# Kernel optimization log

Hardware: AMD Instinct MI355X
Metric: run time of the kernel (lower is better)

The kernel has to match this reference:

```python
import jax, jax.numpy as jnp
import numpy as np

D_INPUT, D_MODEL, D_STATE, D_DISCR, KER = 1024, 2048, 16, 128, 4

def setup_inputs() -> dict:
    key = jax.random.key(0)
    ks = jax.random.split(key, 10)
    sc = lambda fan_in: 1.0 / np.sqrt(fan_in)
    seq = jax.random.normal(ks[0], (2, 1024, D_INPUT), dtype=jnp.float32)
    W_in = jax.random.uniform(ks[1], (2 * D_MODEL, D_INPUT), jnp.float32, -sc(D_INPUT), sc(D_INPUT))
    W_out = jax.random.uniform(ks[2], (D_INPUT, D_MODEL), jnp.float32, -sc(D_MODEL), sc(D_MODEL))
    W_sB = jax.random.uniform(ks[3], (D_STATE, D_MODEL), jnp.float32, -sc(D_MODEL), sc(D_MODEL))
    W_sC = jax.random.uniform(ks[4], (D_STATE, D_MODEL), jnp.float32, -sc(D_MODEL), sc(D_MODEL))
    W_sD1 = jax.random.uniform(ks[5], (D_DISCR, D_MODEL), jnp.float32, -sc(D_MODEL), sc(D_MODEL))
    W_sD2 = jax.random.uniform(ks[6], (D_MODEL, D_DISCR), jnp.float32, -sc(D_DISCR), sc(D_DISCR))
    conv_w = jax.random.uniform(ks[7], (D_MODEL, 1, KER), jnp.float32, -sc(KER), sc(KER))
    conv_b = jax.random.uniform(ks[8], (D_MODEL,), jnp.float32, -sc(KER), sc(KER))
    A_param = jnp.tile(jnp.arange(1, D_STATE + 1, dtype=jnp.float32), (D_MODEL, 1))
    D_param = jnp.ones((D_MODEL,), dtype=jnp.float32)
    return dict(seq=seq, W_in=W_in, W_out=W_out, W_sB=W_sB, W_sC=W_sC,
                W_sD1=W_sD1, W_sD2=W_sD2, conv_w=conv_w, conv_b=conv_b,
                A_param=A_param, D_param=D_param)

def _mamba_fwd(seq, W_in, W_out, W_sB, W_sC, W_sD1, W_sD2, conv_w, conv_b, A_param, D_param):
    b, l, _ = seq.shape
    ab = seq @ W_in.T                                   # [b,l,2*dm]
    a, g = jnp.split(ab, 2, axis=-1)
    # causal depthwise conv: torch pads ker-1 both sides then trims [..., :l]
    x = jnp.swapaxes(a, 1, 2)                           # [b,dm,l]
    y = jax.lax.conv_general_dilated(
        x, conv_w, window_strides=(1,), padding=[(KER - 1, 0)],
        dimension_numbers=('NCH', 'OIH', 'NCH'), feature_group_count=D_MODEL)
    y = y + conv_b[None, :, None]
    a = jax.nn.silu(jnp.swapaxes(y, 1, 2))              # [b,l,dm]
    # SSM
    B = a @ W_sB.T                                      # [b,l,s]
    C = a @ W_sC.T                                      # [b,l,s]
    s_delta = jax.nn.softplus(D_param + (a @ W_sD1.T) @ W_sD2.T)  # [b,l,dm]
    expA = jnp.exp(-A_param)                            # [dm,s]
    A_bar = expA[None, None] * s_delta[..., None]       # [b,l,dm,s]
    X_bar = B[:, :, None, :] * s_delta[..., None] * a[..., None]  # [b,l,dm,s]
    A_t = jnp.moveaxis(A_bar, 1, 0)                     # [l,b,dm,s]
    X_t = jnp.moveaxis(X_bar, 1, 0)
    h0 = jnp.zeros((b, D_MODEL, D_STATE), dtype=seq.dtype)
    def step(h, ax):
        At, Xt = ax
        h = At * h + Xt
        return h, h
    _, hid = jax.lax.scan(step, h0, (A_t, X_t))         # hid: [l,b,dm,s]
    out_ssm = jnp.einsum('lbds,lbs->lbd', hid, jnp.moveaxis(C, 1, 0))
    out_ssm = jnp.moveaxis(out_ssm, 0, 1) + D_param * a # [b,l,dm]
    out = (out_ssm * jax.nn.silu(g)) @ W_out.T          # [b,l,d_input]
    return out

def reference(seq, W_in, W_out, W_sB, W_sC, W_sD1, W_sD2, conv_w, conv_b, A_param, D_param):
    return _mamba_fwd(seq, W_in, W_out, W_sB, W_sC, W_sD1, W_sD2, conv_w, conv_b, A_param, D_param)
```

## Files before the change

kernel.cpp:

```cpp
#include <hip/hip_runtime.h>
#include <math.h>

#define DI 1024
#define DM 2048
#define DS 16
#define LSEQ 1024
#define NB 2
#define NTOK (NB * LSEQ)
#define TC 128
#define WU 32
#define LDU 164
#define NRP 161
#define ZLD 68

typedef unsigned short ushort_t;
typedef __attribute__((ext_vector_type(8))) short short8;
typedef __attribute__((ext_vector_type(4))) float f32x4;

__device__ __forceinline__ float bf2f(ushort_t u) {
    union { unsigned u; float f; } c; c.u = (unsigned)u << 16; return c.f;
}
__device__ __forceinline__ ushort_t f2bf(float f) {
    union { float f; unsigned u; } c; c.f = f;
    unsigned r = c.u + 0x7FFFu + ((c.u >> 16) & 1u);
    return (ushort_t)(r >> 16);
}

__device__ __forceinline__ void gload16(const void* g, void* l) {
    __builtin_amdgcn_global_load_lds(
        (const __attribute__((address_space(1))) void*)g,
        (__attribute__((address_space(3))) void*)l, 16, 0, 0);
}

template<int CTRL>
__device__ __forceinline__ float dpp_mv(float v) {
    int r = __builtin_amdgcn_update_dpp(0, __builtin_bit_cast(int, v), CTRL, 0xF, 0xF, true);
    return __builtin_bit_cast(float, r);
}
__device__ __forceinline__ float sum4(float v) {
    v += dpp_mv<0xB1>(v);
    v += dpp_mv<0x4E>(v);
    return v;
}

__device__ __forceinline__ void cvt4(const float* __restrict__ in,
                                     ushort_t* __restrict__ out, int q) {
    float4 v = ((const float4*)in)[q];
    ushort4 o;
    o.x = f2bf(v.x); o.y = f2bf(v.y); o.z = f2bf(v.z); o.w = f2bf(v.w);
    ((ushort4*)out)[q] = o;
}

__global__ __launch_bounds__(256) void prep(
    const float* __restrict__ seq, const float* __restrict__ W_in,
    const float* __restrict__ W_out, const float* __restrict__ W_sD2,
    const float* __restrict__ Wb, const float* __restrict__ Wc,
    const float* __restrict__ Wd1,
    ushort_t* __restrict__ seq_bf, ushort_t* __restrict__ W_in_bf,
    ushort_t* __restrict__ W_out_bf, ushort_t* __restrict__ W_sD2_bf,
    ushort_t* __restrict__ wbcd)
{
    int q = blockIdx.x * 256 + threadIdx.x;
    if (q < 524288)        cvt4(seq,   seq_bf,   q);
    else if (q < 1572864)  cvt4(W_in,  W_in_bf,  q - 524288);
    else if (q < 2097152)  cvt4(W_out, W_out_bf, q - 1572864);
    else if (q < 2162688)  cvt4(W_sD2, W_sD2_bf, q - 2097152);
    else {
        int p = q - 2162688;
        int idx = p * 4;
        int row = idx >> 11, col = idx & (DM - 1);
        float4 v = make_float4(0.f, 0.f, 0.f, 0.f);
        if (row < 16)       v = *(const float4*)&Wb[row * DM + col];
        else if (row < 32)  v = *(const float4*)&Wc[(row - 16) * DM + col];
        else if (row < 160) v = *(const float4*)&Wd1[(row - 32) * DM + col];
        ushort4 o;
        o.x = f2bf(v.x); o.y = f2bf(v.y); o.z = f2bf(v.z); o.w = f2bf(v.w);
        ((ushort4*)wbcd)[p] = o;
    }
}

template<int TM, int EPI>
__global__ __launch_bounds__(256) void gemm_bt(
    const ushort_t* __restrict__ A, const ushort_t* __restrict__ B,
    void* __restrict__ Cout, int K, int lda, int ldb, int ldc,
    const float* __restrict__ bias, void* __restrict__ Cpart, size_t pstride)
{
    constexpr int MF = TM / 32;
    constexpr int ASZ = TM * 32;
    constexpr int BSZ = 128 * 32;
    __shared__ ushort_t As[2 * ASZ];
    __shared__ ushort_t Bs[2 * BSZ];
    const int tid = threadIdx.x;
    const int lane = tid & 63;
    const int wv = tid >> 6;
    const int wr = wv >> 1, wc = wv & 1;

    const int gx = gridDim.x, gy = gridDim.y;
    const int nwg = gx * gy;
    const int orig = blockIdx.y * gx + blockIdx.x;
    const int q8 = nwg >> 3, r8 = nwg & 7;
    const int xcd = orig & 7, i8 = orig >> 3;
    const int wg = ((xcd < r8) ? xcd * (q8 + 1) : r8 * (q8 + 1) + (xcd - r8) * q8) + i8;
    const int bm = (wg / gx) * TM, bn = (wg % gx) * 128;

    int kbeg = 0, kend = K;
    if (EPI == 5) { int ks = K / gridDim.z; kbeg = blockIdx.z * ks; kend = kbeg + ks; }

    f32x4 acc[MF][4];
#pragma unroll
    for (int m = 0; m < MF; ++m)
#pragma unroll
        for (int n = 0; n < 4; ++n) acc[m][n] = (f32x4){0.f, 0.f, 0.f, 0.f};

    const int r_lo = lane >> 2;
    const int s_l = lane & 3;
    const int row0 = wv * 16 + r_lo;
    const int row1 = 64 + wv * 16 + r_lo;
    const int sg0 = s_l ^ ((row0 >> 1) & 3);
    const int sg1 = s_l ^ ((row1 >> 1) & 3);
    const ushort_t* gA0 = A + (size_t)(bm + row0) * lda + sg0 * 8;
    const ushort_t* gA1 = A + (size_t)(bm + row1) * lda + sg1 * 8;
    const ushort_t* gB0 = B + (size_t)(bn + row0) * ldb + sg0 * 8;
    const ushort_t* gB1 = B + (size_t)(bn + row1) * ldb + sg1 * 8;
    const int lA0o = (wv * 16) * 32;
    const int lA1o = ((TM == 128 ? 64 : 0) + wv * 16) * 32;
    const int lB0o = (wv * 16) * 32;
    const int lB1o = (64 + wv * 16) * 32;

    gload16(gA0 + kbeg, &As[lA0o]);
    if (TM == 128) gload16(gA1 + kbeg, &As[lA1o]);
    gload16(gB0 + kbeg, &Bs[lB0o]);
    gload16(gB1 + kbeg, &Bs[lB1o]);
    __syncthreads();

    int cur = 0;
    for (int k = kbeg; k < kend; k += 32) {
        const int nxt = cur ^ 1;
        if (k + 32 < kend) {
            gload16(gA0 + k + 32, &As[nxt * ASZ + lA0o]);
            if (TM == 128) gload16(gA1 + k + 32, &As[nxt * ASZ + lA1o]);
            gload16(gB0 + k + 32, &Bs[nxt * BSZ + lB0o]);
            gload16(gB1 + k + 32, &Bs[nxt * BSZ + lB1o]);
        }
        const int ca = cur * ASZ, cb = cur * BSZ;
        short8 af[MF], bfr[4];
#pragma unroll
        for (int m = 0; m < MF; ++m) {
            int row = wr * (TM / 2) + m * 16 + (lane & 15);
            int sl = (lane >> 4) ^ ((row >> 1) & 3);
            af[m] = *(const short8*)&As[ca + row * 32 + sl * 8];
        }
#pragma unroll
        for (int n = 0; n < 4; ++n) {
            int row = wc * 64 + n * 16 + (lane & 15);
            int sl = (lane >> 4) ^ ((row >> 1) & 3);
            bfr[n] = *(const short8*)&Bs[cb + row * 32 + sl * 8];
        }
#pragma unroll
        for (int m = 0; m < MF; ++m)
#pragma unroll
            for (int n = 0; n < 4; ++n)
                acc[m][n] = __builtin_amdgcn_mfma_f32_16x16x32_bf16(af[m], bfr[n], acc[m][n], 0, 0, 0);
        __syncthreads();
        cur = nxt;
    }

    const int orow = bm + wr * (TM / 2) + ((lane >> 4) << 2);
    const int ocol = bn + wc * 64 + (lane & 15);
#pragma unroll
    for (int m = 0; m < MF; ++m)
#pragma unroll
        for (int n = 0; n < 4; ++n) {
            int col = ocol + n * 16;
#pragma unroll
            for (int r = 0; r < 4; ++r) {
                int row = orow + m * 16 + r;
                float v = acc[m][n][r];
                if (EPI == 3) {
                    v += bias[col];
                    v = (v > 20.f) ? v : log1pf(__expf(v));
                    ((ushort_t*)Cout)[(size_t)row * ldc + col] = f2bf(v);
                } else if (EPI == 1) {
                    ((ushort_t*)Cout)[(size_t)row * ldc + col] = f2bf(v);
                } else if (EPI == 5) {
                    ((ushort_t*)Cpart + (size_t)blockIdx.z * pstride)[(size_t)row * ldc + col] = f2bf(v);
                } else {
                    ((float*)Cout)[(size_t)row * ldc + col] = v;
                }
            }
        }
}

__global__ __launch_bounds__(256) void reduce_bcd(const ushort_t* __restrict__ part,
                                                  ushort_t* __restrict__ outh)
{
    int q = blockIdx.x * 256 + threadIdx.x;
    float sx = 0.f, sy = 0.f, sz = 0.f, sw = 0.f;
#pragma unroll
    for (int z = 0; z < 8; ++z) {
        ushort4 v = ((const ushort4*)part)[q + z * 131072];
        sx += bf2f(v.x); sy += bf2f(v.y); sz += bf2f(v.z); sw += bf2f(v.w);
    }
    ushort4 o;
    o.x = f2bf(sx); o.y = f2bf(sy); o.z = f2bf(sz); o.w = f2bf(sw);
    ((ushort4*)outh)[q] = o;
}

__global__ __launch_bounds__(256) void reduce_out(const ushort_t* __restrict__ part,
                                                  float* __restrict__ out)
{
    int q = blockIdx.x * 256 + threadIdx.x;
    float sx = 0.f, sy = 0.f, sz = 0.f, sw = 0.f;
#pragma unroll
    for (int z = 0; z < 4; ++z) {
        ushort4 v = ((const ushort4*)part)[q + z * 524288];
        sx += bf2f(v.x); sy += bf2f(v.y); sz += bf2f(v.z); sw += bf2f(v.w);
    }
    float4 o; o.x = sx; o.y = sy; o.z = sz; o.w = sw;
    ((float4*)out)[q] = o;
}

__global__ __launch_bounds__(256) void conv_silu(const ushort_t* __restrict__ ab,
                                                 const float* __restrict__ w,
                                                 const float* __restrict__ bias,
                                                 ushort_t* __restrict__ outh) {
    const int bt = blockIdx.x;
    const int b = bt >> 10, t = bt & (LSEQ - 1);
    const int d = threadIdx.x * 8;

    float wv[8][4];
#pragma unroll
    for (int j = 0; j < 8; ++j) {
        float4 tw = *(const float4*)&w[(d + j) * 4];
        wv[j][0] = tw.x; wv[j][1] = tw.y; wv[j][2] = tw.z; wv[j][3] = tw.w;
    }
    float accv[8];
    {
        float4 b0 = *(const float4*)&bias[d];
        float4 b1 = *(const float4*)&bias[d + 4];
        accv[0] = b0.x; accv[1] = b0.y; accv[2] = b0.z; accv[3] = b0.w;
        accv[4] = b1.x; accv[5] = b1.y; accv[6] = b1.z; accv[7] = b1.w;
    }
#pragma unroll
    for (int k = 0; k < 4; ++k) {
        int tt = t + k - 3;
        if (tt >= 0) {
            short8 av = *(const short8*)&ab[(size_t)(b * LSEQ + tt) * (2 * DM) + d];
#pragma unroll
            for (int j = 0; j < 8; ++j)
                accv[j] = fmaf(bf2f((ushort_t)av[j]), wv[j][k], accv[j]);
        }
    }
    short8 o;
#pragma unroll
    for (int j = 0; j < 8; ++j) {
        float s = accv[j] / (1.f + __expf(-accv[j]));
        o[j] = (short)f2bf(s);
    }
    *(short8*)&outh[(size_t)bt * DM + d] = o;
}

__global__ __launch_bounds__(256) void scan_win(
    const ushort_t* __restrict__ sdel, const ushort_t* __restrict__ aconv,
    const ushort_t* __restrict__ bcd1, const ushort_t* __restrict__ ab,
    const float* __restrict__ A_param, const float* __restrict__ D_param,
    ushort_t* __restrict__ z)
{
    __shared__ ushort_t Ssh[64 * LDU];
    __shared__ ushort_t Vsh[64 * LDU];
    __shared__ float    Bq[4 * NRP * 4];
    __shared__ float    Cq[4 * NRP * 4];
    __shared__ ushort_t Zsh[TC * ZLD];

    const int tid = threadIdx.x;
    const int d0 = blockIdx.x * 64;
    const int c = blockIdx.y, b = blockIdx.z;
    const int nw = (c == 0) ? 0 : WU;
    const int nrows = nw + TC;
    const int tok0 = b * LSEQ + c * TC - nw;
    const int tokout0 = b * LSEQ + c * TC;

    for (int j = tid; j < (nrows / 4) * 32; j += 256) {
        int a = j & 1;
        int r = j >> 1;
        int cq = (r & 15) * 4;
        int row4 = (r >> 4) * 4;
        const ushort_t* src = (a ? aconv : sdel) + (size_t)(tok0 + row4) * DM + d0 + cq;
        ushort4 v0 = *(const ushort4*)(src);
        ushort4 v1 = *(const ushort4*)(src + DM);
        ushort4 v2 = *(const ushort4*)(src + 2 * DM);
        ushort4 v3 = *(const ushort4*)(src + 3 * DM);
        ushort_t* dst = (a ? Vsh : Ssh) + row4;
        *(ushort4*)(dst + (cq + 0) * LDU) = make_ushort4(v0.x, v1.x, v2.x, v3.x);
        *(ushort4*)(dst + (cq + 1) * LDU) = make_ushort4(v0.y, v1.y, v2.y, v3.y);
        *(ushort4*)(dst + (cq + 2) * LDU) = make_ushort4(v0.z, v1.z, v2.z, v3.z);
        *(ushort4*)(dst + (cq + 3) * LDU) = make_ushort4(v0.w, v1.w, v2.w, v3.w);
    }
    for (int j = tid; j < nrows * 8; j += 256) {
        int row = j >> 3, p = j & 7, g = p & 3;
        const ushort_t* src = bcd1 + (size_t)(tok0 + row) * 256 + ((p < 4) ? 4 * g : 16 + 4 * g);
        ushort4 v = *(const ushort4*)src;
        float4 f = make_float4(bf2f(v.x), bf2f(v.y), bf2f(v.z), bf2f(v.w));
        float* dst = ((p < 4) ? Bq : Cq) + (g * NRP + row) * 4;
        *(float4*)dst = f;
    }
    __syncthreads();

    const int q = tid & 3, dl = tid >> 2;
    const int d = d0 + dl;
    float4 av4 = *(const float4*)&A_param[d * DS + 4 * q];
    const float ea0 = __expf(-av4.x), ea1 = __expf(-av4.y);
    const float ea2 = __expf(-av4.z), ea3 = __expf(-av4.w);
    const float Dp = D_param[d];
    float h0 = 0.f, h1 = 0.f, h2 = 0.f, h3 = 0.f;

#define SCAN_STEP_WU(SD, AV, BI) {                                    \
        float sd = (SD), x = sd * (AV);                               \
        float4 Bv = *(const float4*)&Bq[(q * NRP + (BI)) * 4];        \
        h0 = fmaf(sd * ea0, h0, x * Bv.x);                           \
        h1 = fmaf(sd * ea1, h1, x * Bv.y);                           \
        h2 = fmaf(sd * ea2, h2, x * Bv.z);                           \
        h3 = fmaf(sd * ea3, h3, x * Bv.w); }

    for (int i4 = 0; i4 < nw; i4 += 4) {
        ushort4 sdv = *(const ushort4*)&Ssh[dl * LDU + i4];
        ushort4 avv = *(const ushort4*)&Vsh[dl * LDU + i4];
        SCAN_STEP_WU(bf2f(sdv.x), bf2f(avv.x), i4 + 0);
        SCAN_STEP_WU(bf2f(sdv.y), bf2f(avv.y), i4 + 1);
        SCAN_STEP_WU(bf2f(sdv.z), bf2f(avv.z), i4 + 2);
        SCAN_STEP_WU(bf2f(sdv.w), bf2f(avv.w), i4 + 3);
    }

#define SCAN_STEP_OUT(SD, AV, BI, RV) {                               \
        float sd = (SD), av_ = (AV), x = sd * av_;                    \
        float4 Bv = *(const float4*)&Bq[(q * NRP + (BI)) * 4];        \
        float4 Cv = *(const float4*)&Cq[(q * NRP + (BI)) * 4];        \
        h0 = fmaf(sd * ea0, h0, x * Bv.x);                           \
        h1 = fmaf(sd * ea1, h1, x * Bv.y);                           \
        h2 = fmaf(sd * ea2, h2, x * Bv.z);                           \
        h3 = fmaf(sd * ea3, h3, x * Bv.w);                           \
        float r = h0 * Cv.x;                                          \
        r = fmaf(h1, Cv.y, r); r = fmaf(h2, Cv.z, r);                 \
        r = fmaf(h3, Cv.w, r);                                        \
        r = sum4(r);                                                  \
        RV = fmaf(Dp, av_, r); }

    for (int i4 = nw; i4 < nrows; i4 += 4) {
        ushort4 sdv = *(const ushort4*)&Ssh[dl * LDU + i4];
        ushort4 avv = *(const ushort4*)&Vsh[dl * LDU + i4];
        float rv0, rv1, rv2, rv3;
        SCAN_STEP_OUT(bf2f(sdv.x), bf2f(avv.x), i4 + 0, rv0);
        SCAN_STEP_OUT(bf2f(sdv.y), bf2f(avv.y), i4 + 1, rv1);
        SCAN_STEP_OUT(bf2f(sdv.z), bf2f(avv.z), i4 + 2, rv2);
        SCAN_STEP_OUT(bf2f(sdv.w), bf2f(avv.w), i4 + 3, rv3);
        float rvq = (q == 0) ? rv0 : (q == 1) ? rv1 : (q == 2) ? rv2 : rv3;
        int io = i4 - nw;
        Zsh[(io + q) * ZLD + dl] = f2bf(rvq);
    }
    __syncthreads();
    for (int j = tid; j < TC * 16; j += 256) {
        int row = j >> 4, cq = (j & 15) * 4;
        ushort4 ov = *(const ushort4*)&Zsh[row * ZLD + cq];
        ushort4 gv = *(const ushort4*)&ab[(size_t)(tokout0 + row) * (2 * DM) + DM + d0 + cq];
        ushort4 o;
        float g0 = bf2f(gv.x), g1 = bf2f(gv.y), g2 = bf2f(gv.z), g3 = bf2f(gv.w);
        o.x = f2bf(bf2f(ov.x) * (g0 / (1.f + __expf(-g0))));
        o.y = f2bf(bf2f(ov.y) * (g1 / (1.f + __expf(-g1))));
        o.z = f2bf(bf2f(ov.z) * (g2 / (1.f + __expf(-g2))));
        o.w = f2bf(bf2f(ov.w) * (g3 / (1.f + __expf(-g3))));
        *(ushort4*)&z[(size_t)(tokout0 + row) * DM + d0 + cq] = o;
    }
#undef SCAN_STEP_WU
#undef SCAN_STEP_OUT
}

extern "C" void kernel_launch(void* const* d_in, const int* in_sizes, int n_in,
                              void* d_out, int out_size, void* d_ws, size_t ws_size,
                              hipStream_t stream) {
    const float* seq    = (const float*)d_in[0];
    const float* W_in   = (const float*)d_in[1];
    const float* W_out  = (const float*)d_in[2];
    const float* W_sB   = (const float*)d_in[3];
    const float* W_sC   = (const float*)d_in[4];
    const float* W_sD1  = (const float*)d_in[5];
    const float* W_sD2  = (const float*)d_in[6];
    const float* conv_w = (const float*)d_in[7];
    const float* conv_b = (const float*)d_in[8];
    const float* A_par  = (const float*)d_in[9];
    const float* D_par  = (const float*)d_in[10];
    float* out = (float*)d_out;

    char* ws = (char*)d_ws;
    const size_t MiB = 1024 * 1024;
    ushort_t* ab_bf    = (ushort_t*)(ws);
    ushort_t* part_out = (ushort_t*)(ws);
    ushort_t* aconv_h  = (ushort_t*)(ws + 16 * MiB);
    ushort_t* sdel_h   = (ushort_t*)(ws + 24 * MiB);
    ushort_t* W_out_bf = (ushort_t*)(ws + 32 * MiB);
    ushort_t* bcd1     = (ushort_t*)(ws + 36 * MiB);
    ushort_t* W_sD2_bf = (ushort_t*)(ws + 37 * MiB);
    ushort_t* Wbcd     = (ushort_t*)(ws + 37 * MiB + 512*1024);
    ushort_t* seq_bf   = (ushort_t*)(ws + 39 * MiB);
    ushort_t* W_in_bf  = (ushort_t*)(ws + 43 * MiB);
    ushort_t* partK    = (ushort_t*)(ws + 43 * MiB);
    ushort_t* z_bf     = (ushort_t*)(ws + 63 * MiB);

    dim3 blk(256);

    prep<<<dim3(8960), blk, 0, stream>>>(seq, W_in, W_out, W_sD2, W_sB, W_sC, W_sD1,
                                         seq_bf, W_in_bf, W_out_bf, W_sD2_bf, Wbcd);

    gemm_bt<64, 1><<<dim3(32, 32), blk, 0, stream>>>(seq_bf, W_in_bf, ab_bf, 1024, DI, DI, 2 * DM, nullptr, nullptr, 0);

    conv_silu<<<dim3(NTOK), blk, 0, stream>>>(ab_bf, conv_w, conv_b, aconv_h);

    gemm_bt<64, 5><<<dim3(2, 32, 8), blk, 0, stream>>>(aconv_h, Wbcd, nullptr, DM, DM, DM, 256, nullptr, partK, 2048 * 256);

    reduce_bcd<<<dim3(512), blk, 0, stream>>>(partK, bcd1);

    gemm_bt<64, 3><<<dim3(16, 32), blk, 0, stream>>>(bcd1 + 32, W_sD2_bf, sdel_h, 128, 256, 128, DM, D_par, nullptr, 0);

    scan_win<<<dim3(DM / 64, LSEQ / TC, NB), blk, 0, stream>>>(
        sdel_h, aconv_h, bcd1, ab_bf, A_par, D_par, z_bf);

    gemm_bt<64, 5><<<dim3(8, 32, 4), blk, 0, stream>>>(z_bf, W_out_bf, nullptr, DM, DM, DM, DI, nullptr, part_out, 2048 * 1024);

    reduce_out<<<dim3(2048), blk, 0, stream>>>(part_out, out);
}
```

Before: 138.5 us.

## Fuse split-K partial reduction into delta GEMM A-load and scan B/C load

```diff
diff --git a/kernel.cpp b/kernel.cpp
--- a/kernel.cpp
+++ b/kernel.cpp
@@ -12,6 +12,7 @@
 #define LDU 164
 #define NRP 161
 #define ZLD 68
+#define NZ 8
 
 typedef unsigned short ushort_t;
 typedef __attribute__((ext_vector_type(8))) short short8;
@@ -79,7 +80,7 @@
     }
 }
 
-template<int TM, int EPI>
+template<int TM, int EPI, bool ASUM8 = false>
 __global__ __launch_bounds__(256) void gemm_bt(
     const ushort_t* __restrict__ A, const ushort_t* __restrict__ B,
     void* __restrict__ Cout, int K, int lda, int ldb, int ldc,
@@ -118,51 +119,100 @@
     const int row1 = 64 + wv * 16 + r_lo;
     const int sg0 = s_l ^ ((row0 >> 1) & 3);
     const int sg1 = s_l ^ ((row1 >> 1) & 3);
-    const ushort_t* gA0 = A + (size_t)(bm + row0) * lda + sg0 * 8;
-    const ushort_t* gA1 = A + (size_t)(bm + row1) * lda + sg1 * 8;
     const ushort_t* gB0 = B + (size_t)(bn + row0) * ldb + sg0 * 8;
     const ushort_t* gB1 = B + (size_t)(bn + row1) * ldb + sg1 * 8;
-    const int lA0o = (wv * 16) * 32;
-    const int lA1o = ((TM == 128 ? 64 : 0) + wv * 16) * 32;
     const int lB0o = (wv * 16) * 32;
     const int lB1o = (64 + wv * 16) * 32;
 
-    gload16(gA0 + kbeg, &As[lA0o]);
-    if (TM == 128) gload16(gA1 + kbeg, &As[lA1o]);
-    gload16(gB0 + kbeg, &Bs[lB0o]);
-    gload16(gB1 + kbeg, &Bs[lB1o]);
-    __syncthreads();
-
-    int cur = 0;
-    for (int k = kbeg; k < kend; k += 32) {
-        const int nxt = cur ^ 1;
-        if (k + 32 < kend) {
-            gload16(gA0 + k + 32, &As[nxt * ASZ + lA0o]);
-            if (TM == 128) gload16(gA1 + k + 32, &As[nxt * ASZ + lA1o]);
-            gload16(gB0 + k + 32, &Bs[nxt * BSZ + lB0o]);
-            gload16(gB1 + k + 32, &Bs[nxt * BSZ + lB1o]);
+    if constexpr (ASUM8) {
+        const int r = tid >> 2, s = tid & 3;
+        const int sg = s ^ ((r >> 1) & 3);
+        const ushort_t* gA = A + (size_t)(bm + r) * lda + sg * 8;
+        for (int k = kbeg; k < kend; k += 32) {
+            gload16(gB0 + k, &Bs[lB0o]);
+            gload16(gB1 + k, &Bs[lB1o]);
+            float fa[8];
+#pragma unroll
+            for (int j = 0; j < 8; ++j) fa[j] = 0.f;
+#pragma unroll
+            for (int zz = 0; zz < NZ; ++zz) {
+                const ushort_t* p = gA + (size_t)zz * pstride + k;
+                ushort4 v0 = *(const ushort4*)p;
+                ushort4 v1 = *(const ushort4*)(p + 4);
+                fa[0] += bf2f(v0.x); fa[1] += bf2f(v0.y);
+                fa[2] += bf2f(v0.z); fa[3] += bf2f(v0.w);
+                fa[4] += bf2f(v1.x); fa[5] += bf2f(v1.y);
+                fa[6] += bf2f(v1.z); fa[7] += bf2f(v1.w);
+            }
+            ushort4 o0, o1;
+            o0.x = f2bf(fa[0]); o0.y = f2bf(fa[1]); o0.z = f2bf(fa[2]); o0.w = f2bf(fa[3]);
+            o1.x = f2bf(fa[4]); o1.y = f2bf(fa[5]); o1.z = f2bf(fa[6]); o1.w = f2bf(fa[7]);
+            *(ushort4*)&As[r * 32 + s * 8] = o0;
+            *(ushort4*)&As[r * 32 + s * 8 + 4] = o1;
+            __syncthreads();
+            short8 af[MF], bfr[4];
+#pragma unroll
+            for (int m = 0; m < MF; ++m) {
+                int row = wr * (TM / 2) + m * 16 + (lane & 15);
+                int sl = (lane >> 4) ^ ((row >> 1) & 3);
+                af[m] = *(const short8*)&As[row * 32 + sl * 8];
+            }
+#pragma unroll
+            for (int n = 0; n < 4; ++n) {
+                int row = wc * 64 + n * 16 + (lane & 15);
+                int sl = (lane >> 4) ^ ((row >> 1) & 3);
+                bfr[n] = *(const short8*)&Bs[row * 32 + sl * 8];
+            }
+#pragma unroll
+            for (int m = 0; m < MF; ++m)
+#pragma unroll
+                for (int n = 0; n < 4; ++n)
+                    acc[m][n] = __builtin_amdgcn_mfma_f32_16x16x32_bf16(af[m], bfr[n], acc[m][n], 0, 0, 0);
+            __syncthreads();
         }
-        const int ca = cur * ASZ, cb = cur * BSZ;
-        short8 af[MF], bfr[4];
-#pragma unroll
-        for (int m = 0; m < MF; ++m) {
-            int row = wr * (TM / 2) + m * 16 + (lane & 15);
-            int sl = (lane >> 4) ^ ((row >> 1) & 3);
-            af[m] = *(const short8*)&As[ca + row * 32 + sl * 8];
+    } else {
+        const ushort_t* gA0 = A + (size_t)(bm + row0) * lda + sg0 * 8;
+        const ushort_t* gA1 = A + (size_t)(bm + row1) * lda + sg1 * 8;
+        const int lA0o = (wv * 16) * 32;
+        const int lA1o = ((TM == 128 ? 64 : 0) + wv * 16) * 32;
+
+        gload16(gA0 + kbeg, &As[lA0o]);
+        if (TM == 128) gload16(gA1 + kbeg, &As[lA1o]);
+        gload16(gB0 + kbeg, &Bs[lB0o]);
+        gload16(gB1 + kbeg, &Bs[lB1o]);
+        __syncthreads();
+
+        int cur = 0;
+        for (int k = kbeg; k < kend; k += 32) {
+            const int nxt = cur ^ 1;
+            if (k + 32 < kend) {
+                gload16(gA0 + k + 32, &As[nxt * ASZ + lA0o]);
+                if (TM == 128) gload16(gA1 + k + 32, &As[nxt * ASZ + lA1o]);
+                gload16(gB0 + k + 32, &Bs[nxt * BSZ + lB0o]);
+                gload16(gB1 + k + 32, &Bs[nxt * BSZ + lB1o]);
+            }
+            const int ca = cur * ASZ, cb = cur * BSZ;
+            short8 af[MF], bfr[4];
+#pragma unroll
+            for (int m = 0; m < MF; ++m) {
+                int row = wr * (TM / 2) + m * 16 + (lane & 15);
+                int sl = (lane >> 4) ^ ((row >> 1) & 3);
+                af[m] = *(const short8*)&As[ca + row * 32 + sl * 8];
+            }
+#pragma unroll
+            for (int n = 0; n < 4; ++n) {
+                int row = wc * 64 + n * 16 + (lane & 15);
+                int sl = (lane >> 4) ^ ((row >> 1) & 3);
+                bfr[n] = *(const short8*)&Bs[cb + row * 32 + sl * 8];
+            }
+#pragma unroll
+            for (int m = 0; m < MF; ++m)
+#pragma unroll
+                for (int n = 0; n < 4; ++n)
+                    acc[m][n] = __builtin_amdgcn_mfma_f32_16x16x32_bf16(af[m], bfr[n], acc[m][n], 0, 0, 0);
+            __syncthreads();
+            cur = nxt;
         }
-#pragma unroll
-        for (int n = 0; n < 4; ++n) {
-            int row = wc * 64 + n * 16 + (lane & 15);
-            int sl = (lane >> 4) ^ ((row >> 1) & 3);
-            bfr[n] = *(const short8*)&Bs[cb + row * 32 + sl * 8];
-        }
-#pragma unroll
-        for (int m = 0; m < MF; ++m)
-#pragma unroll
-            for (int n = 0; n < 4; ++n)
-                acc[m][n] = __builtin_amdgcn_mfma_f32_16x16x32_bf16(af[m], bfr[n], acc[m][n], 0, 0, 0);
-        __syncthreads();
-        cur = nxt;
     }
 
     const int orow = bm + wr * (TM / 2) + ((lane >> 4) << 2);
@@ -178,7 +228,7 @@
                 float v = acc[m][n][r];
                 if (EPI == 3) {
                     v += bias[col];
-                    v = (v > 20.f) ? v : log1pf(__expf(v));
+                    v = (v > 20.f) ? v : __logf(1.f + __expf(v));
                     ((ushort_t*)Cout)[(size_t)row * ldc + col] = f2bf(v);
                 } else if (EPI == 1) {
                     ((ushort_t*)Cout)[(size_t)row * ldc + col] = f2bf(v);
@@ -191,21 +241,6 @@
         }
 }
 
-__global__ __launch_bounds__(256) void reduce_bcd(const ushort_t* __restrict__ part,
-                                                  ushort_t* __restrict__ outh)
-{
-    int q = blockIdx.x * 256 + threadIdx.x;
-    float sx = 0.f, sy = 0.f, sz = 0.f, sw = 0.f;
-#pragma unroll
-    for (int z = 0; z < 8; ++z) {
-        ushort4 v = ((const ushort4*)part)[q + z * 131072];
-        sx += bf2f(v.x); sy += bf2f(v.y); sz += bf2f(v.z); sw += bf2f(v.w);
-    }
-    ushort4 o;
-    o.x = f2bf(sx); o.y = f2bf(sy); o.z = f2bf(sz); o.w = f2bf(sw);
-    ((ushort4*)outh)[q] = o;
-}
-
 __global__ __launch_bounds__(256) void reduce_out(const ushort_t* __restrict__ part,
                                                   float* __restrict__ out)
 {
@@ -262,7 +297,7 @@
 
 __global__ __launch_bounds__(256) void scan_win(
     const ushort_t* __restrict__ sdel, const ushort_t* __restrict__ aconv,
-    const ushort_t* __restrict__ bcd1, const ushort_t* __restrict__ ab,
+    const ushort_t* __restrict__ partK, const ushort_t* __restrict__ ab,
     const float* __restrict__ A_param, const float* __restrict__ D_param,
     ushort_t* __restrict__ z)
 {
@@ -298,11 +333,15 @@
     }
     for (int j = tid; j < nrows * 8; j += 256) {
         int row = j >> 3, p = j & 7, g = p & 3;
-        const ushort_t* src = bcd1 + (size_t)(tok0 + row) * 256 + ((p < 4) ? 4 * g : 16 + 4 * g);
-        ushort4 v = *(const ushort4*)src;
-        float4 f = make_float4(bf2f(v.x), bf2f(v.y), bf2f(v.z), bf2f(v.w));
+        size_t off = (size_t)(tok0 + row) * 256 + ((p < 4) ? 4 * g : 16 + 4 * g);
+        float fx = 0.f, fy = 0.f, fz = 0.f, fw = 0.f;
+#pragma unroll
+        for (int zz = 0; zz < NZ; ++zz) {
+            ushort4 v = *(const ushort4*)&partK[(size_t)zz * (2048 * 256) + off];
+            fx += bf2f(v.x); fy += bf2f(v.y); fz += bf2f(v.z); fw += bf2f(v.w);
+        }
         float* dst = ((p < 4) ? Bq : Cq) + (g * NRP + row) * 4;
-        *(float4*)dst = f;
+        *(float4*)dst = make_float4(fx, fy, fz, fw);
     }
     __syncthreads();
 
@@ -397,7 +436,6 @@
     ushort_t* aconv_h  = (ushort_t*)(ws + 16 * MiB);
     ushort_t* sdel_h   = (ushort_t*)(ws + 24 * MiB);
     ushort_t* W_out_bf = (ushort_t*)(ws + 32 * MiB);
-    ushort_t* bcd1     = (ushort_t*)(ws + 36 * MiB);
     ushort_t* W_sD2_bf = (ushort_t*)(ws + 37 * MiB);
     ushort_t* Wbcd     = (ushort_t*)(ws + 37 * MiB + 512*1024);
     ushort_t* seq_bf   = (ushort_t*)(ws + 39 * MiB);
@@ -416,12 +454,10 @@
 
     gemm_bt<64, 5><<<dim3(2, 32, 8), blk, 0, stream>>>(aconv_h, Wbcd, nullptr, DM, DM, DM, 256, nullptr, partK, 2048 * 256);
 
-    reduce_bcd<<<dim3(512), blk, 0, stream>>>(partK, bcd1);
-
-    gemm_bt<64, 3><<<dim3(16, 32), blk, 0, stream>>>(bcd1 + 32, W_sD2_bf, sdel_h, 128, 256, 128, DM, D_par, nullptr, 0);
+    gemm_bt<64, 3, true><<<dim3(16, 32), blk, 0, stream>>>(partK + 32, W_sD2_bf, sdel_h, 128, 256, 128, DM, D_par, nullptr, 2048 * 256);
 
     scan_win<<<dim3(DM / 64, LSEQ / TC, NB), blk, 0, stream>>>(
-        sdel_h, aconv_h, bcd1, ab_bf, A_par, D_par, z_bf);
+        sdel_h, aconv_h, partK, ab_bf, A_par, D_par, z_bf);
 
     gemm_bt<64, 5><<<dim3(8, 32, 4), blk, 0, stream>>>(z_bf, W_out_bf, nullptr, DM, DM, DM, DI, nullptr, part_out, 2048 * 1024);
 
```

New measurement: 128.2 us. -7.4%, faster.
